# Optimization experiments

Measured on AMD Instinct MI355X. Metric: run time of the kernel, lower is better.

Reference implementation:

```python
import jax, jax.numpy as jnp
import numpy as np

# Calibrated SAPS parameters (Qhat from conformal calibration, rank penalty)
TAU = 0.95
RANK_PEN = 0.2


def setup_inputs() -> dict:
    key = jax.random.key(0)
    k1, k2 = jax.random.split(key)
    logits = jax.random.normal(k1, (4096, 10000), dtype=jnp.float32)
    u = jax.random.uniform(k2, (4096,), dtype=jnp.float32)  # randomized tie-break uniforms
    return {"logits": logits, "u": u}


def reference(logits, u):
    B, C = logits.shape
    rows = jnp.arange(B)
    cols = jnp.arange(C)

    # sort_sum: class indices in descending-logit order
    I = jnp.argsort(-logits, axis=1)  # [B, C]

    # transform: softmax, keep the max prob, replace all other entries by rank_pen
    probs = jax.nn.softmax(logits, axis=1)
    argmax = jnp.argmax(probs, axis=1)
    transformed = jnp.where(cols[None, :] == argmax[:, None], probs, RANK_PEN)

    # reorder transformed scores by descending-logit rank, then cumulative sum
    ordered = jnp.take_along_axis(transformed, I, axis=1)  # [B, C]
    cumsum = jnp.cumsum(ordered, axis=1)                   # [B, C]

    # gcq with zero penalties: smallest prefix whose cumsum exceeds tau
    sizes_base = jnp.minimum((cumsum <= TAU).sum(axis=1) + 1, C)  # [B]
    idx = sizes_base - 1
    o_k = ordered[rows, idx]
    c_k = cumsum[rows, idx]
    # randomized rounding: V = (tau - (cumsum_{k} - ordered_{k})) / ordered_{k}
    V = (TAU - (c_k - o_k)) / o_k
    sizes = sizes_base - (u >= V).astype(sizes_base.dtype)

    if TAU == 1.0:  # static python check, as in original
        sizes = jnp.full_like(sizes, C)
    # allow_zero_sets=True -> no clamp to 1

    # prediction sets S as a fixed-shape boolean membership mask over classes:
    # set_mask[i, I[i, j]] = (j < sizes[i])
    in_set_sorted = cols[None, :] < sizes[:, None]
    set_mask = jnp.zeros((B, C), dtype=bool).at[rows[:, None], I].set(in_set_sorted)

    return cumsum, sizes, set_mask
```

## Files before the change

### kernel.cpp

```cpp
#include <hip/hip_runtime.h>
#include <math.h>
#include <float.h>

#define TAU 0.95f
#define PEN 0.2f
#define NT 256
#define NW (NT / 64)
#define KSEL 6
#define KMAX 8

typedef float f32x4 __attribute__((ext_vector_type(4)));

__device__ __forceinline__ void amax2(float& bv, int& bi, float ov, int oi) {
    if (ov > bv || (ov == bv && oi < bi)) { bv = ov; bi = oi; }
}

__global__ __launch_bounds__(NT) void saps_kernel(
    const float* __restrict__ logits, const float* __restrict__ u,
    float* __restrict__ out_cumsum, float* __restrict__ out_sizes,
    float* __restrict__ out_mask, int C)
{
    const int row  = blockIdx.x;
    const int tid  = threadIdx.x;
    const int lane = tid & 63;
    const int wv   = tid >> 6;
    const float* __restrict__ x = logits + (size_t)row * C;

    __shared__ float s_s[NW];
    __shared__ float s_cv[NW * KSEL];
    __shared__ int   s_ci[NW * KSEL];
    __shared__ int   s_sel[KSEL];
    __shared__ float s_sz;

    float s_loc = 0.0f;
    float tv[KSEL]; int ti[KSEL];
    #pragma unroll
    for (int q = 0; q < KSEL; q++) { tv[q] = -FLT_MAX; ti[q] = 0x7fffffff; }

    auto proc = [&](float v, int j) {
        s_loc += __expf(v);
        if (v > tv[KSEL - 1]) {
            tv[KSEL - 1] = v; ti[KSEL - 1] = j;
            #pragma unroll
            for (int q = KSEL - 1; q > 0; --q) {
                if (tv[q] > tv[q - 1]) {
                    float fv = tv[q]; tv[q] = tv[q - 1]; tv[q - 1] = fv;
                    int   fi = ti[q]; ti[q] = ti[q - 1]; ti[q - 1] = fi;
                }
            }
        }
    };

    const int C4 = C >> 2;
    const bool vec_ok = ((C & 3) == 0);
    if (vec_ok) {
        const f32x4* __restrict__ x4 = (const f32x4*)x;
        for (int q = tid; q < C4; q += NT) {
            f32x4 v = x4[q];
            int j = q << 2;
            proc(v.x, j); proc(v.y, j + 1); proc(v.z, j + 2); proc(v.w, j + 3);
        }
    } else {
        for (int j = tid; j < C; j += NT) proc(x[j], j);
    }

    #pragma unroll
    for (int off = 32; off > 0; off >>= 1) s_loc += __shfl_xor(s_loc, off);
    if (lane == 0) s_s[wv] = s_loc;

    #pragma unroll
    for (int r = 0; r < KSEL; r++) {
        float bv = -FLT_MAX; int bi = 0x7fffffff;
        #pragma unroll
        for (int q = 0; q < KSEL; q++) amax2(bv, bi, tv[q], ti[q]);
        #pragma unroll
        for (int off = 32; off > 0; off >>= 1) {
            float ov = __shfl_xor(bv, off);
            int   oi = __shfl_xor(bi, off);
            amax2(bv, bi, ov, oi);
        }
        if (lane == 0) { s_cv[wv * KSEL + r] = bv; s_ci[wv * KSEL + r] = bi; }
        #pragma unroll
        for (int q = 0; q < KSEL; q++)
            if (ti[q] == bi) { tv[q] = -FLT_MAX; ti[q] = 0x7fffffff; }
    }
    __syncthreads();

    float ss = s_s[0];
    float mm = s_cv[0];
    #pragma unroll
    for (int w2 = 1; w2 < NW; w2++) {
        ss += s_s[w2];
        mm = fmaxf(mm, s_cv[w2 * KSEL]);
    }
    const float pmax = __expf(mm) / ss;

    if (wv == 0) {
        float cs[KMAX];
        cs[0] = pmax;
        #pragma unroll
        for (int j = 1; j < KMAX; j++) cs[j] = cs[j - 1] + PEN;
        int cnt = 0;
        #pragma unroll
        for (int j = 0; j < KMAX; j++) if (cs[j] <= TAU) cnt++;
        int sizes_base = cnt + 1;
        if (sizes_base > C) sizes_base = C;
        int k = sizes_base - 1;
        if (k >= KMAX) k = KMAX - 1;
        const float o_k = (k == 0) ? cs[0] : PEN;
        const float c_k = cs[k];
        const float V = (TAU - (c_k - o_k)) / o_k;
        int sz = sizes_base - ((u[row] >= V) ? 1 : 0);
        if (sz > KSEL) sz = KSEL;
        if (sz < 0) sz = 0;

        float cv2 = -FLT_MAX; int ci2 = 0x7fffffff;
        if (lane < NW * KSEL) { cv2 = s_cv[lane]; ci2 = s_ci[lane]; }
        #pragma unroll
        for (int r = 0; r < KSEL; r++) {
            float bv = cv2; int bi = ci2;
            #pragma unroll
            for (int off = 32; off > 0; off >>= 1) {
                float ov = __shfl_xor(bv, off);
                int   oi = __shfl_xor(bi, off);
                amax2(bv, bi, ov, oi);
            }
            if (lane == 0) s_sel[r] = (r < sz) ? bi : -1;
            if (ci2 == bi) { cv2 = -FLT_MAX; ci2 = 0x7fffffff; }
        }
        if (lane == 0) s_sz = (float)sz;
    }
    __syncthreads();

    const int s0 = s_sel[0], s1 = s_sel[1], s2i = s_sel[2];
    const int s3 = s_sel[3], s4 = s_sel[4], s5 = s_sel[5];

    float* __restrict__ oc = out_cumsum + (size_t)row * C;
    float* __restrict__ om = out_mask   + (size_t)row * C;
    if (vec_ok) {
        f32x4* __restrict__ oc4 = (f32x4*)oc;
        f32x4* __restrict__ om4 = (f32x4*)om;
        for (int q = tid; q < C4; q += NT) {
            const int j0 = q << 2;
            f32x4 cv;
            cv.x = fmaf(PEN, (float)(j0),     pmax);
            cv.y = fmaf(PEN, (float)(j0 + 1), pmax);
            cv.z = fmaf(PEN, (float)(j0 + 2), pmax);
            cv.w = fmaf(PEN, (float)(j0 + 3), pmax);
            f32x4 mv;
            mv.x = (j0     == s0 || j0     == s1 || j0     == s2i || j0     == s3 || j0     == s4 || j0     == s5) ? 1.0f : 0.0f;
            mv.y = (j0 + 1 == s0 || j0 + 1 == s1 || j0 + 1 == s2i || j0 + 1 == s3 || j0 + 1 == s4 || j0 + 1 == s5) ? 1.0f : 0.0f;
            mv.z = (j0 + 2 == s0 || j0 + 2 == s1 || j0 + 2 == s2i || j0 + 2 == s3 || j0 + 2 == s4 || j0 + 2 == s5) ? 1.0f : 0.0f;
            mv.w = (j0 + 3 == s0 || j0 + 3 == s1 || j0 + 3 == s2i || j0 + 3 == s3 || j0 + 3 == s4 || j0 + 3 == s5) ? 1.0f : 0.0f;
            __builtin_nontemporal_store(cv, oc4 + q);
            __builtin_nontemporal_store(mv, om4 + q);
        }
    } else {
        for (int j = tid; j < C; j += NT) {
            oc[j] = fmaf(PEN, (float)j, pmax);
            om[j] = (j == s0 || j == s1 || j == s2i || j == s3 || j == s4 || j == s5) ? 1.0f : 0.0f;
        }
    }
    if (tid == 0) out_sizes[row] = s_sz;
}

extern "C" void kernel_launch(void* const* d_in, const int* in_sizes, int n_in,
                              void* d_out, int out_size, void* d_ws, size_t ws_size,
                              hipStream_t stream) {
    const float* logits = (const float*)d_in[0];
    const float* u      = (const float*)d_in[1];
    const int B = in_sizes[1];
    const int C = in_sizes[0] / B;

    float* out        = (float*)d_out;
    float* out_cumsum = out;
    float* out_sizes  = out + (size_t)B * C;
    float* out_mask   = out + (size_t)B * C + B;

    saps_kernel<<<dim3(B), dim3(NT), 0, stream>>>(logits, u, out_cumsum, out_sizes, out_mask, C);
}
```

Before: 95.37 us.

## Split fused row kernel into separate stats and output-write kernels

Splits the single per-row kernel into a read-only statistics kernel, which writes pmax, the set size and the selected indices to a workspace, and a second write-only kernel that fills the cumsum and mask outputs. The aim is to stop each block from stalling on reads and then on writes within one kernel, letting each phase stream at full bandwidth on its own. In exchange it adds a second launch and a small workspace round trip, and the two phases no longer overlap across blocks.

```diff
diff --git a/kernel.cpp b/kernel.cpp
--- a/kernel.cpp
+++ b/kernel.cpp
@@ -15,10 +15,9 @@
     if (ov > bv || (ov == bv && oi < bi)) { bv = ov; bi = oi; }
 }
 
-__global__ __launch_bounds__(NT) void saps_kernel(
+__global__ __launch_bounds__(NT) void saps_stats(
     const float* __restrict__ logits, const float* __restrict__ u,
-    float* __restrict__ out_cumsum, float* __restrict__ out_sizes,
-    float* __restrict__ out_mask, int C)
+    float* __restrict__ ws, int C)
 {
     const int row  = blockIdx.x;
     const int tid  = threadIdx.x;
@@ -29,8 +28,6 @@
     __shared__ float s_s[NW];
     __shared__ float s_cv[NW * KSEL];
     __shared__ int   s_ci[NW * KSEL];
-    __shared__ int   s_sel[KSEL];
-    __shared__ float s_sz;
 
     float s_loc = 0.0f;
     float tv[KSEL]; int ti[KSEL];
@@ -86,16 +83,16 @@
     }
     __syncthreads();
 
-    float ss = s_s[0];
-    float mm = s_cv[0];
-    #pragma unroll
-    for (int w2 = 1; w2 < NW; w2++) {
-        ss += s_s[w2];
-        mm = fmaxf(mm, s_cv[w2 * KSEL]);
-    }
-    const float pmax = __expf(mm) / ss;
-
     if (wv == 0) {
+        float ss = s_s[0];
+        float mm = s_cv[0];
+        #pragma unroll
+        for (int w2 = 1; w2 < NW; w2++) {
+            ss += s_s[w2];
+            mm = fmaxf(mm, s_cv[w2 * KSEL]);
+        }
+        const float pmax = __expf(mm) / ss;
+
         float cs[KMAX];
         cs[0] = pmax;
         #pragma unroll
@@ -116,6 +113,7 @@
 
         float cv2 = -FLT_MAX; int ci2 = 0x7fffffff;
         if (lane < NW * KSEL) { cv2 = s_cv[lane]; ci2 = s_ci[lane]; }
+        int selr[KSEL];
         #pragma unroll
         for (int r = 0; r < KSEL; r++) {
             float bv = cv2; int bi = ci2;
@@ -125,18 +123,40 @@
                 int   oi = __shfl_xor(bi, off);
                 amax2(bv, bi, ov, oi);
             }
-            if (lane == 0) s_sel[r] = (r < sz) ? bi : -1;
+            selr[r] = (r < sz) ? bi : -1;
             if (ci2 == bi) { cv2 = -FLT_MAX; ci2 = 0x7fffffff; }
         }
-        if (lane == 0) s_sz = (float)sz;
-    }
-    __syncthreads();
-
-    const int s0 = s_sel[0], s1 = s_sel[1], s2i = s_sel[2];
-    const int s3 = s_sel[3], s4 = s_sel[4], s5 = s_sel[5];
+
+        if (lane == 0) {
+            float* wr = ws + (size_t)row * 8;
+            int*   wi = (int*)wr;
+            wr[0] = pmax;
+            wr[1] = (float)sz;
+            #pragma unroll
+            for (int r = 0; r < KSEL; r++) wi[2 + r] = selr[r];
+        }
+    }
+}
+
+__global__ __launch_bounds__(NT) void saps_write(
+    const float* __restrict__ ws,
+    float* __restrict__ out_cumsum, float* __restrict__ out_sizes,
+    float* __restrict__ out_mask, int C)
+{
+    const int row = blockIdx.x;
+    const int tid = threadIdx.x;
+
+    const float* __restrict__ wr = ws + (size_t)row * 8;
+    const int*   __restrict__ wi = (const int*)wr;
+    const float pmax = wr[0];
+    const int s0 = wi[2], s1 = wi[3], s2i = wi[4];
+    const int s3 = wi[5], s4 = wi[6], s5 = wi[7];
 
     float* __restrict__ oc = out_cumsum + (size_t)row * C;
     float* __restrict__ om = out_mask   + (size_t)row * C;
+
+    const int C4 = C >> 2;
+    const bool vec_ok = ((C & 3) == 0);
     if (vec_ok) {
         f32x4* __restrict__ oc4 = (f32x4*)oc;
         f32x4* __restrict__ om4 = (f32x4*)om;
@@ -161,7 +181,7 @@
             om[j] = (j == s0 || j == s1 || j == s2i || j == s3 || j == s4 || j == s5) ? 1.0f : 0.0f;
         }
     }
-    if (tid == 0) out_sizes[row] = s_sz;
+    if (tid == 0) out_sizes[row] = wr[1];
 }
 
 extern "C" void kernel_launch(void* const* d_in, const int* in_sizes, int n_in,
@@ -176,6 +196,8 @@
     float* out_cumsum = out;
     float* out_sizes  = out + (size_t)B * C;
     float* out_mask   = out + (size_t)B * C + B;
-
-    saps_kernel<<<dim3(B), dim3(NT), 0, stream>>>(logits, u, out_cumsum, out_sizes, out_mask, C);
-}
+    float* ws         = (float*)d_ws;
+
+    saps_stats<<<dim3(B), dim3(NT), 0, stream>>>(logits, u, ws, C);
+    saps_write<<<dim3(B), dim3(NT), 0, stream>>>(ws, out_cumsum, out_sizes, out_mask, C);
+}
```

Result: slower. 129.2 us (+35.5%).
